# Optimization experiments

Hardware: AMD Instinct MI355X
Metric: run time of the kernel (lower is better)

Reference implementation:

```python
import jax, jax.numpy as jnp
import numpy as np

N = 50000      # nodes across the batched graph
E = 400000     # edges
F_IN = 128     # gnn_input_size
H = 3          # num_head
D = 64         # gnn_hidden_size
G = 64         # graphs in batch
P = 64         # pattern_input_size
NEG_GAT = 0.2  # GATv2Conv leaky_relu slope (dgl default)
NEG = 0.01     # nn.LeakyReLU default slope


def setup_inputs() -> dict:
    key = jax.random.key(0)
    ks = jax.random.split(key, 32)
    rn = lambda k, s, sc=0.05: jax.random.normal(k, s, dtype=jnp.float32) * sc
    HD = H * D
    return {
        "inputs": rn(ks[0], (N, F_IN), 1.0),
        "src": jax.random.randint(ks[1], (E,), 0, N),
        "dst": jax.random.randint(ks[2], (E,), 0, N),
        "graph_ids": jnp.sort(jax.random.randint(ks[3], (N,), 0, G)),
        "p1": rn(ks[4], (G, P), 1.0),
        "p2": rn(ks[5], (G, P), 1.0),
        "p3": rn(ks[6], (G, P), 1.0),
        # GATv2 layer params: fc_src, fc_dst, attn vector, bias
        "W1s": rn(ks[7], (F_IN, HD)), "W1d": rn(ks[8], (F_IN, HD)),
        "a1": rn(ks[9], (H, D)), "b1": rn(ks[10], (HD,)),
        "W2s": rn(ks[11], (HD, HD)), "W2d": rn(ks[12], (HD, HD)),
        "a2": rn(ks[13], (H, D)), "b2": rn(ks[14], (HD,)),
        "W3s": rn(ks[15], (HD, HD)), "W3d": rn(ks[16], (HD, HD)),
        "a3": rn(ks[17], (H, D)), "b3": rn(ks[18], (HD,)),
        # pattern branch (forward only uses ex_layer1 for all three inputs)
        "Wex": rn(ks[19], (P, 32)), "bex": rn(ks[20], (32,)),
        "Wpat": rn(ks[21], (96, P)), "bpat": rn(ks[22], (P,)),
        # classifier head
        "Wc1": rn(ks[23], (D + P, 64)), "bc1": rn(ks[24], (64,)),
        "Wc2": rn(ks[25], (64, 32)), "bc2": rn(ks[26], (32,)),
        "Wc3": rn(ks[27], (32, 2)), "bc3": rn(ks[28], (2,)),
    }


def _gatv2(x, src, dst, Ws, Wd, attn, bias):
    # dgl GATv2Conv (share_weights=False): e = a . leaky_relu(Ws x_u + Wd x_v)
    fs = (x @ Ws).reshape(N, H, D)
    fd = (x @ Wd).reshape(N, H, D)
    e = jax.nn.leaky_relu(fs[src] + fd[dst], NEG_GAT)            # [E,H,D]
    logits = jnp.einsum('ehd,hd->eh', e, attn)                   # [E,H]
    m = jax.ops.segment_max(logits, dst, num_segments=N)         # [N,H]
    m = jnp.where(jnp.isfinite(m), m, 0.0)                       # nodes w/o in-edges
    ex = jnp.exp(logits - m[dst])
    denom = jax.ops.segment_sum(ex, dst, num_segments=N)         # [N,H]
    alpha = ex / jnp.maximum(denom, 1e-9)[dst]                   # edge softmax
    out = jax.ops.segment_sum(alpha[:, :, None] * fs[src], dst, num_segments=N)
    return out + bias.reshape(1, H, D)                           # [N,H,D]


def reference(inputs, src, dst, graph_ids, p1, p2, p3,
              W1s, W1d, a1, b1, W2s, W2d, a2, b2, W3s, W3d, a3, b3,
              Wex, bex, Wpat, bpat, Wc1, bc1, Wc2, bc2, Wc3, bc3):
    h = _gatv2(inputs, src, dst, W1s, W1d, a1, b1).reshape(N, H * D)
    h = _gatv2(h, src, dst, W2s, W2d, a2, b2).reshape(N, H * D)
    h = _gatv2(h, src, dst, W3s, W3d, a3, b3).mean(axis=1)       # [N,D]
    # dgl.mean_nodes: per-graph mean over nodes
    sums = jax.ops.segment_sum(h, graph_ids, num_segments=G)
    cnts = jax.ops.segment_sum(jnp.ones((N,), h.dtype), graph_ids, num_segments=G)
    gnn_out = sums / jnp.maximum(cnts, 1.0)[:, None]             # [G,D]
    # pattern branch (ex_layer1 applied to all three, as in source)
    px = jnp.concatenate([p1 @ Wex + bex, p2 @ Wex + bex, p3 @ Wex + bex], axis=1)
    px = jax.nn.leaky_relu(px @ Wpat + bpat, NEG)                # [G,P]
    x = jnp.concatenate([gnn_out, px], axis=1)                   # [G,D+P]
    x = jax.nn.leaky_relu(x @ Wc1 + bc1, NEG)
    x = jax.nn.leaky_relu(x @ Wc2 + bc2, NEG)
    return x @ Wc3 + bc3                                         # [G,2]
```

## Files before the change

kernel.cpp:

```cpp
#include <hip/hip_runtime.h>
#include <cstdint>
#include <cstddef>

#define NN 50000
#define EE 400000
#define FIN 128
#define HH 3
#define DD 64
#define GG 64
#define PP 64
#define HD 192

typedef short bf16x8 __attribute__((ext_vector_type(8)));
typedef float f32x4 __attribute__((ext_vector_type(4)));
typedef unsigned int u32x2 __attribute__((ext_vector_type(2)));

__device__ inline int wsumi(int v) {
#pragma unroll
    for (int m = 32; m > 0; m >>= 1) v += __shfl_xor(v, m, 64);
    return v;
}

__device__ inline float bf2f(unsigned short u) {
    union { unsigned int i; float f; } x; x.i = ((unsigned int)u) << 16; return x.f;
}
__device__ inline unsigned short f2bf(float f) {
    union { float f; unsigned int i; } x; x.f = f;
    unsigned int r = x.i + 0x7FFFu + ((x.i >> 16) & 1u);
    return (unsigned short)(r >> 16);
}

__device__ inline void unp2(unsigned int w, float& lo, float& hi) {
    union { unsigned int i; float f; } x;
    x.i = w << 16;          lo = x.f;
    x.i = w & 0xFFFF0000u;  hi = x.f;
}
__device__ inline void load4(const unsigned short* p, float* o) {
    u32x2 w = *(const u32x2*)p;
    unp2(w[0], o[0], o[1]);
    unp2(w[1], o[2], o[3]);
}

__device__ inline void loadrow(const unsigned short* __restrict__ FS, int u, int col,
                               float f[3][4]) {
    size_t bu = (size_t)u * HD + col;
#pragma unroll
    for (int h = 0; h < 3; h++) load4(&FS[bu + h * 64], f[h]);
}

__global__ void k_count(const int* __restrict__ dst, int* __restrict__ counts) {
    int e = blockIdx.x * 256 + threadIdx.x;
    if (e < EE) atomicAdd(&counts[dst[e]], 1);
}

__global__ void k_scan_block(const int* __restrict__ in, int* __restrict__ out,
                             int* __restrict__ bsums) {
    __shared__ int tmp[1024];
    int tid = threadIdx.x;
    int i = blockIdx.x * 1024 + tid;
    int v = (i < NN) ? in[i] : 0;
    tmp[tid] = v;
    __syncthreads();
    for (int off = 1; off < 1024; off <<= 1) {
        int t = (tid >= off) ? tmp[tid - off] : 0;
        __syncthreads();
        tmp[tid] += t;
        __syncthreads();
    }
    if (i < NN) out[i] = tmp[tid] - v;
    if (tid == 1023) bsums[blockIdx.x] = tmp[1023];
}

__global__ void k_scan_add(int* __restrict__ row_ptr, const int* __restrict__ bsums, int nb) {
    __shared__ int sbase;
    int tid = threadIdx.x;
    if (tid < 64) {
        int v = (tid < blockIdx.x) ? bsums[tid] : 0;
        v = wsumi(v);
        if (tid == 0) sbase = v;
    }
    __syncthreads();
    int i = blockIdx.x * 1024 + tid;
    if (i < NN) row_ptr[i] += sbase;
    else if (i == NN) row_ptr[NN] = EE;
}

__global__ void k_scatter(const int* __restrict__ src, const int* __restrict__ dst,
                          const int* __restrict__ row_ptr, int* __restrict__ cursor,
                          int* __restrict__ csr_src) {
    int e = blockIdx.x * 256 + threadIdx.x;
    if (e >= EE) return;
    int v = dst[e];
    int pos = row_ptr[v] + atomicAdd(&cursor[v], 1);
    csr_src[pos] = src[e];
}

__device__ inline void pack_one(const float* __restrict__ W, unsigned short* __restrict__ WP,
                                int id, int Kc) {
    int lane = id & 63;
    int kc = (id >> 6) % Kc;
    int ct = (id >> 6) / Kc;
    int n = ct * 16 + (lane & 15);
    int kb = kc * 32 + (lane >> 4) * 8;
#pragma unroll
    for (int j = 0; j < 8; j++)
        WP[(unsigned)id * 8 + j] = f2bf(W[(unsigned)(kb + j) * HD + n]);
}

#define IDS128 (12 * 4 * 64)
#define IDS192 (12 * 6 * 64)
__global__ void k_pack_all(const float* W1s, const float* W1d,
                           const float* W2s, const float* W2d,
                           const float* W3s, const float* W3d,
                           unsigned short* P1s, unsigned short* P1d,
                           unsigned short* P2s, unsigned short* P2d,
                           unsigned short* P3s, unsigned short* P3d) {
    int idx = blockIdx.x * 256 + threadIdx.x;
    if (idx < IDS128) { pack_one(W1s, P1s, idx, 4); return; }
    idx -= IDS128;
    if (idx < IDS128) { pack_one(W1d, P1d, idx, 4); return; }
    idx -= IDS128;
    if (idx < IDS192) { pack_one(W2s, P2s, idx, 6); return; }
    idx -= IDS192;
    if (idx < IDS192) { pack_one(W2d, P2d, idx, 6); return; }
    idx -= IDS192;
    if (idx < IDS192) { pack_one(W3s, P3s, idx, 6); return; }
    idx -= IDS192;
    if (idx < IDS192) { pack_one(W3d, P3d, idx, 6); return; }
}

template <int K, bool BF16IN>
__global__ __launch_bounds__(256) void k_gemm_mfma(const void* __restrict__ Xin,
                                                   const unsigned short* __restrict__ WPs,
                                                   const unsigned short* __restrict__ WPd,
                                                   unsigned short* __restrict__ FS,
                                                   unsigned short* __restrict__ FD) {
    constexpr int Kc = K / 32;
    __shared__ unsigned short smem[64 * 392];
    unsigned short (*xs)[K + 8] = (unsigned short (*)[K + 8])smem;
    unsigned short (*cs)[392]   = (unsigned short (*)[392])smem;
    int tid = threadIdx.x;
    int row0 = blockIdx.x * 64;

    if (BF16IN) {
        const unsigned short* XB = (const unsigned short*)Xin;
        for (int c = tid; c < 64 * K / 8; c += 256) {
            int r = c / (K / 8), kk = (c - r * (K / 8)) * 8;
            int row = row0 + r; if (row > NN - 1) row = NN - 1;
            *(bf16x8*)&xs[r][kk] = *(const bf16x8*)&XB[(unsigned)(row * K + kk)];
        }
    } else {
        const float* X = (const float*)Xin;
        for (int c = tid; c < 64 * K / 4; c += 256) {
            int r = c / (K / 4), k4 = (c - r * (K / 4)) * 4;
            int row = row0 + r; if (row > NN - 1) row = NN - 1;
            f32x4 v = *(const f32x4*)&X[(unsigned)(row * K + k4)];
            xs[r][k4 + 0] = f2bf(v[0]);
            xs[r][k4 + 1] = f2bf(v[1]);
            xs[r][k4 + 2] = f2bf(v[2]);
            xs[r][k4 + 3] = f2bf(v[3]);
        }
    }
    __syncthreads();

    int lane = tid & 63, wv = tid >> 6;
    int m = lane & 15, quad = lane >> 4;
    f32x4 acc[4][6];
#pragma unroll
    for (int s = 0; s < 4; s++)
#pragma unroll
        for (int t = 0; t < 6; t++) acc[s][t] = (f32x4){0.f, 0.f, 0.f, 0.f};

    for (int kc = 0; kc < Kc; kc++) {
        bf16x8 b[6];
#pragma unroll
        for (int t = 0; t < 6; t++) {
            int ct = wv * 6 + t;
            const unsigned short* wp = (ct < 12) ? WPs : WPd;
            int c = (ct < 12) ? ct : ct - 12;
            b[t] = *(const bf16x8*)&wp[(unsigned)(((c * Kc + kc) * 64 + lane) * 8)];
        }
#pragma unroll
        for (int s = 0; s < 4; s++) {
            bf16x8 a = *(const bf16x8*)&xs[s * 16 + m][kc * 32 + quad * 8];
#pragma unroll
            for (int t = 0; t < 6; t++)
                acc[s][t] = __builtin_amdgcn_mfma_f32_16x16x32_bf16(a, b[t], acc[s][t], 0, 0, 0);
        }
    }
    __syncthreads();
#pragma unroll
    for (int s = 0; s < 4; s++)
#pragma unroll
        for (int t = 0; t < 6; t++) {
            int ct = wv * 6 + t;
#pragma unroll
            for (int r = 0; r < 4; r++)
                cs[s * 16 + quad * 4 + r][ct * 16 + m] = f2bf(acc[s][t][r]);
        }
    __syncthreads();
#pragma unroll
    for (int it = 0; it < 12; it++) {
        int c = tid + it * 256;
        int hm = c / 1536;
        int cc = c - hm * 1536;
        int row = cc / 24, ch = cc - row * 24;
        int grow = row0 + row;
        if (grow < NN) {
            unsigned short* OUT = hm ? FD : FS;
            *(bf16x8*)&OUT[(unsigned)(grow * HD + ch * 8)] =
                *(const bf16x8*)&cs[row][hm * 192 + ch * 8];
        }
    }
}

template <bool FINAL>
__global__ __launch_bounds__(256) void k_node_gat(const int* __restrict__ row_ptr,
                                                  const int* __restrict__ csr_src,
                                                  const unsigned short* __restrict__ FS,
                                                  const unsigned short* __restrict__ FD,
                                                  const float* __restrict__ A,
                                                  const float* __restrict__ Bv,
                                                  unsigned short* __restrict__ XB,
                                                  float* __restrict__ H64) {
    int tid = threadIdx.x;
    int grp = tid >> 4, sub = tid & 15;
    int node = blockIdx.x * 16 + grp;
    int col = sub * 4;

    float a[3][4];
#pragma unroll
    for (int h = 0; h < 3; h++) {
        f32x4 av = *(const f32x4*)&A[h * 64 + col];
#pragma unroll
        for (int j = 0; j < 4; j++) a[h][j] = av[j];
    }

    int lo = row_ptr[node], hi = row_ptr[node + 1];

    float g[3][4];
#pragma unroll
    for (int h = 0; h < 3; h++) load4(&FD[(size_t)node * HD + h * 64 + col], g[h]);

    float r[3][4];
#pragma unroll
    for (int h = 0; h < 3; h++)
#pragma unroll
        for (int j = 0; j < 4; j++) r[h][j] = 0.f;
    float d0 = 0.f, d1 = 0.f, d2 = 0.f;

    auto accum = [&](const float f[3][4]) {
        float p0 = 0.f, p1 = 0.f, p2 = 0.f;
#pragma unroll
        for (int j = 0; j < 4; j++) {
            float s0 = f[0][j] + g[0][j]; s0 = fmaxf(s0, 0.2f * s0); p0 += s0 * a[0][j];
            float s1 = f[1][j] + g[1][j]; s1 = fmaxf(s1, 0.2f * s1); p1 += s1 * a[1][j];
            float s2 = f[2][j] + g[2][j]; s2 = fmaxf(s2, 0.2f * s2); p2 += s2 * a[2][j];
        }
#pragma unroll
        for (int m = 8; m > 0; m >>= 1) {
            p0 += __shfl_xor(p0, m, 64);
            p1 += __shfl_xor(p1, m, 64);
            p2 += __shfl_xor(p2, m, 64);
        }
        float w0 = __expf(p0), w1 = __expf(p1), w2 = __expf(p2);
#pragma unroll
        for (int j = 0; j < 4; j++) {
            r[0][j] += w0 * f[0][j];
            r[1][j] += w1 * f[1][j];
            r[2][j] += w2 * f[2][j];
        }
        d0 += w0; d1 += w1; d2 += w2;
    };

    if (hi > lo) {
        int last = hi - 1;
        float fA[3][4], fB[3][4], fC[3][4];
        loadrow(FS, csr_src[lo], col, fA);
        loadrow(FS, csr_src[lo + 1 <= last ? lo + 1 : last], col, fB);
        for (int e = lo; e < hi; e += 3) {
            int eC = e + 2 <= last ? e + 2 : last;
            int eA = e + 3 <= last ? e + 3 : last;
            int eB = e + 4 <= last ? e + 4 : last;
            int uC = csr_src[eC], uA = csr_src[eA], uB = csr_src[eB];
            loadrow(FS, uC, col, fC);
            accum(fA);
            loadrow(FS, uA, col, fA);
            if (e + 1 < hi) accum(fB);
            loadrow(FS, uB, col, fB);
            if (e + 2 < hi) accum(fC);
        }
    }

    float b[3][4];
#pragma unroll
    for (int h = 0; h < 3; h++) {
        f32x4 bv = *(const f32x4*)&Bv[h * 64 + col];
#pragma unroll
        for (int j = 0; j < 4; j++) b[h][j] = bv[j];
    }

    float q0 = fmaxf(d0, 1e-9f), q1 = fmaxf(d1, 1e-9f), q2 = fmaxf(d2, 1e-9f);
    if (FINAL) {
        f32x4 m;
#pragma unroll
        for (int j = 0; j < 4; j++)
            m[j] = (r[0][j] / q0 + b[0][j] + r[1][j] / q1 + b[1][j] +
                    r[2][j] / q2 + b[2][j]) * (1.f / 3.f);
        *(f32x4*)&H64[(size_t)node * 64 + col] = m;
    } else {
        float qq[3] = {q0, q1, q2};
#pragma unroll
        for (int h = 0; h < 3; h++) {
            unsigned short o0 = f2bf(r[h][0] / qq[h] + b[h][0]);
            unsigned short o1 = f2bf(r[h][1] / qq[h] + b[h][1]);
            unsigned short o2 = f2bf(r[h][2] / qq[h] + b[h][2]);
            unsigned short o3 = f2bf(r[h][3] / qq[h] + b[h][3]);
            u32x2 w;
            w[0] = (unsigned)o0 | ((unsigned)o1 << 16);
            w[1] = (unsigned)o2 | ((unsigned)o3 << 16);
            *(u32x2*)&XB[(size_t)node * HD + h * 64 + col] = w;
        }
    }
}

__global__ __launch_bounds__(256) void k_graph_mean(const float* __restrict__ H64,
                                                    const int* __restrict__ gids,
                                                    float* __restrict__ gsum,
                                                    int* __restrict__ gcnt) {
    int g = blockIdx.x >> 2, q = blockIdx.x & 3;
    int lo, hi;
    {
        int a = 0, b = NN;
        while (a < b) { int m = (a + b) >> 1; if (gids[m] < g) a = m + 1; else b = m; }
        lo = a;
        b = NN;
        while (a < b) { int m = (a + b) >> 1; if (gids[m] < g + 1) a = m + 1; else b = m; }
        hi = a;
    }
    int len = hi - lo;
    int qlen = (len + 3) >> 2;
    int s = lo + q * qlen;
    int e = s + qlen; if (e > hi) e = hi;
    int lane = threadIdx.x & 63, wv = threadIdx.x >> 6;

    float acc = 0.f;
    for (int v = s + wv; v < e; v += 4)
        acc += H64[(size_t)v * 64 + lane];
    __shared__ float red[4][64];
    red[wv][lane] = acc;
    __syncthreads();
    if (wv == 0) {
        float t = red[0][lane] + red[1][lane] + red[2][lane] + red[3][lane];
        if (e > s) {
            atomicAdd(&gsum[g * 64 + lane], t);
            if (lane == 0) atomicAdd(&gcnt[g], e - s);
        }
    }
}

__global__ __launch_bounds__(128) void k_head(const float* __restrict__ gsum, const int* __restrict__ gcnt,
                                              const float* __restrict__ p1, const float* __restrict__ p2,
                                              const float* __restrict__ p3,
                                              const float* __restrict__ Wex, const float* __restrict__ bex,
                                              const float* __restrict__ Wpat, const float* __restrict__ bpat,
                                              const float* __restrict__ Wc1, const float* __restrict__ bc1,
                                              const float* __restrict__ Wc2, const float* __restrict__ bc2,
                                              const float* __restrict__ Wc3, const float* __restrict__ bc3,
                                              float* __restrict__ out) {
    int g = blockIdx.x;
    int tid = threadIdx.x;
    __shared__ float pbuf[192];
    __shared__ float ex[96], xc[128], t1[64], t2[32];

    if (tid < 64)       pbuf[tid] = p1[g * 64 + tid];
    else if (tid < 128) pbuf[tid] = p2[g * 64 + tid - 64];
    if (tid < 64)       pbuf[128 + tid] = p3[g * 64 + tid];
    if (tid >= 64 && tid < 128)
        xc[tid - 64] = gsum[g * 64 + tid - 64] / fmaxf((float)gcnt[g], 1.f);
    __syncthreads();
    if (tid < 96) {
        int jj = tid & 31;
        const float* pp = &pbuf[(tid >> 5) * 64];
        float acc = bex[jj];
        for (int k = 0; k < 64; k++) acc += pp[k] * Wex[k * 32 + jj];
        ex[tid] = acc;
    }
    __syncthreads();
    if (tid < 64) {
        float acc = bpat[tid];
        for (int k = 0; k < 96; k++) acc += ex[k] * Wpat[k * 64 + tid];
        xc[64 + tid] = acc > 0.f ? acc : 0.01f * acc;
    }
    __syncthreads();
    if (tid < 64) {
        float acc = bc1[tid];
        for (int k = 0; k < 128; k++) acc += xc[k] * Wc1[k * 64 + tid];
        t1[tid] = acc > 0.f ? acc : 0.01f * acc;
    }
    __syncthreads();
    if (tid < 32) {
        float acc = bc2[tid];
        for (int k = 0; k < 64; k++) acc += t1[k] * Wc2[k * 32 + tid];
        t2[tid] = acc > 0.f ? acc : 0.01f * acc;
    }
    __syncthreads();
    if (tid < 2) {
        float acc = bc3[tid];
        for (int k = 0; k < 32; k++) acc += t2[k] * Wc3[k * 2 + tid];
        out[g * 2 + tid] = acc;
    }
}

extern "C" void kernel_launch(void* const* d_in, const int* in_sizes, int n_in,
                              void* d_out, int out_size, void* d_ws, size_t ws_size,
                              hipStream_t stream) {
    const float* X0  = (const float*)d_in[0];
    const int*   src = (const int*)d_in[1];
    const int*   dst = (const int*)d_in[2];
    const int*   gid = (const int*)d_in[3];
    const float* p1  = (const float*)d_in[4];
    const float* p2  = (const float*)d_in[5];
    const float* p3  = (const float*)d_in[6];
    const float* W1s = (const float*)d_in[7],  *W1d = (const float*)d_in[8];
    const float* a1  = (const float*)d_in[9],  *b1  = (const float*)d_in[10];
    const float* W2s = (const float*)d_in[11], *W2d = (const float*)d_in[12];
    const float* a2  = (const float*)d_in[13], *b2  = (const float*)d_in[14];
    const float* W3s = (const float*)d_in[15], *W3d = (const float*)d_in[16];
    const float* a3  = (const float*)d_in[17], *b3  = (const float*)d_in[18];
    const float* Wex = (const float*)d_in[19], *bex = (const float*)d_in[20];
    const float* Wpat= (const float*)d_in[21], *bpat= (const float*)d_in[22];
    const float* Wc1 = (const float*)d_in[23], *bc1 = (const float*)d_in[24];
    const float* Wc2 = (const float*)d_in[25], *bc2 = (const float*)d_in[26];
    const float* Wc3 = (const float*)d_in[27], *bc3 = (const float*)d_in[28];
    float* out = (float*)d_out;

    char* ws = (char*)d_ws;
    size_t off = 0;
    auto alloc = [&](size_t bytes) -> char* {
        char* p = ws + off;
        off = (off + bytes + 255) & ~(size_t)255;
        return p;
    };
    unsigned short* FS = (unsigned short*)alloc((size_t)NN * HD * 2);
    unsigned short* FD = (unsigned short*)alloc((size_t)NN * HD * 2);
    unsigned short* XB = (unsigned short*)alloc((size_t)NN * HD * 2);
    float*          H64= (float*)alloc((size_t)NN * 64 * 4);
    unsigned short* P1s = (unsigned short*)alloc((size_t)192 * 192 * 2);
    unsigned short* P1d = (unsigned short*)alloc((size_t)192 * 192 * 2);
    unsigned short* P2s = (unsigned short*)alloc((size_t)192 * 192 * 2);
    unsigned short* P2d = (unsigned short*)alloc((size_t)192 * 192 * 2);
    unsigned short* P3s = (unsigned short*)alloc((size_t)192 * 192 * 2);
    unsigned short* P3d = (unsigned short*)alloc((size_t)192 * 192 * 2);
    int* row_ptr = (int*)alloc((size_t)(NN + 1) * 4);
    int* csr_src = (int*)alloc((size_t)EE * 4);
    int* bsums   = (int*)alloc(64 * 4);
    char* zbase = ws + off;
    int*   counts = (int*)alloc((size_t)NN * 4);
    int*   cursor = (int*)alloc((size_t)NN * 4);
    float* gsum   = (float*)alloc((size_t)GG * 64 * 4);
    int*   gcnt   = (int*)alloc((size_t)GG * 4);
    size_t zbytes = (size_t)((ws + off) - zbase);

    hipMemsetAsync(zbase, 0, zbytes, stream);

    int ebl = (EE + 255) / 256;
    int nb  = (NN + 1023) / 1024;
    k_count<<<ebl, 256, 0, stream>>>(dst, counts);
    k_scan_block<<<nb, 1024, 0, stream>>>(counts, row_ptr, bsums);
    k_scan_add<<<nb, 1024, 0, stream>>>(row_ptr, bsums, nb);
    k_scatter<<<ebl, 256, 0, stream>>>(src, dst, row_ptr, cursor, csr_src);
    {
        int total = 2 * IDS128 + 4 * IDS192;
        k_pack_all<<<(total + 255) / 256, 256, 0, stream>>>(W1s, W1d, W2s, W2d, W3s, W3d,
                                                            P1s, P1d, P2s, P2d, P3s, P3d);
    }

    int gblk = (NN + 63) / 64;
    int nblk = NN / 16;

    k_gemm_mfma<128, false><<<gblk, 256, 0, stream>>>(X0, P1s, P1d, FS, FD);
    k_node_gat<false><<<nblk, 256, 0, stream>>>(row_ptr, csr_src, FS, FD, a1, b1, XB, nullptr);
    k_gemm_mfma<192, true><<<gblk, 256, 0, stream>>>(XB, P2s, P2d, FS, FD);
    k_node_gat<false><<<nblk, 256, 0, stream>>>(row_ptr, csr_src, FS, FD, a2, b2, XB, nullptr);
    k_gemm_mfma<192, true><<<gblk, 256, 0, stream>>>(XB, P3s, P3d, FS, FD);
    k_node_gat<true><<<nblk, 256, 0, stream>>>(row_ptr, csr_src, FS, FD, a3, b3, nullptr, H64);

    k_graph_mean<<<GG * 4, 256, 0, stream>>>(H64, gid, gsum, gcnt);
    k_head<<<GG, 128, 0, stream>>>(gsum, gcnt, p1, p2, p3, Wex, bex, Wpat, bpat,
                                   Wc1, bc1, Wc2, bc2, Wc3, bc3, out);
}
```

Baseline: 377.7 us.

## Split GEMM into src/dst halves, fuse count with pack, use shuffle-based scan

The MFMA projection kernel now computes the source and destination outputs in two sequential halves. This halves the accumulator registers and the LDS staging buffer, and launch bounds request 4 blocks per SM to raise occupancy. The cost is loading the input tile into LDS twice. Separately, the edge-count and weight-pack kernels are merged into one launch, and the block scan uses wave shuffles instead of a barrier-heavy shared-memory Hillis-Steele scan.

New measurement: 368.0 us, median of 3. 2.5% less time.

```diff
diff --git a/kernel.cpp b/kernel.cpp
--- a/kernel.cpp
+++ b/kernel.cpp
@@ -10,6 +10,7 @@
 #define GG 64
 #define PP 64
 #define HD 192
+#define EBL 1563
 
 typedef short bf16x8 __attribute__((ext_vector_type(8)));
 typedef float f32x4 __attribute__((ext_vector_type(4)));
@@ -46,53 +47,6 @@
     size_t bu = (size_t)u * HD + col;
 #pragma unroll
     for (int h = 0; h < 3; h++) load4(&FS[bu + h * 64], f[h]);
-}
-
-__global__ void k_count(const int* __restrict__ dst, int* __restrict__ counts) {
-    int e = blockIdx.x * 256 + threadIdx.x;
-    if (e < EE) atomicAdd(&counts[dst[e]], 1);
-}
-
-__global__ void k_scan_block(const int* __restrict__ in, int* __restrict__ out,
-                             int* __restrict__ bsums) {
-    __shared__ int tmp[1024];
-    int tid = threadIdx.x;
-    int i = blockIdx.x * 1024 + tid;
-    int v = (i < NN) ? in[i] : 0;
-    tmp[tid] = v;
-    __syncthreads();
-    for (int off = 1; off < 1024; off <<= 1) {
-        int t = (tid >= off) ? tmp[tid - off] : 0;
-        __syncthreads();
-        tmp[tid] += t;
-        __syncthreads();
-    }
-    if (i < NN) out[i] = tmp[tid] - v;
-    if (tid == 1023) bsums[blockIdx.x] = tmp[1023];
-}
-
-__global__ void k_scan_add(int* __restrict__ row_ptr, const int* __restrict__ bsums, int nb) {
-    __shared__ int sbase;
-    int tid = threadIdx.x;
-    if (tid < 64) {
-        int v = (tid < blockIdx.x) ? bsums[tid] : 0;
-        v = wsumi(v);
-        if (tid == 0) sbase = v;
-    }
-    __syncthreads();
-    int i = blockIdx.x * 1024 + tid;
-    if (i < NN) row_ptr[i] += sbase;
-    else if (i == NN) row_ptr[NN] = EE;
-}
-
-__global__ void k_scatter(const int* __restrict__ src, const int* __restrict__ dst,
-                          const int* __restrict__ row_ptr, int* __restrict__ cursor,
-                          int* __restrict__ csr_src) {
-    int e = blockIdx.x * 256 + threadIdx.x;
-    if (e >= EE) return;
-    int v = dst[e];
-    int pos = row_ptr[v] + atomicAdd(&cursor[v], 1);
-    csr_src[pos] = src[e];
 }
 
 __device__ inline void pack_one(const float* __restrict__ W, unsigned short* __restrict__ WP,
@@ -109,13 +63,21 @@
 
 #define IDS128 (12 * 4 * 64)
 #define IDS192 (12 * 6 * 64)
-__global__ void k_pack_all(const float* W1s, const float* W1d,
-                           const float* W2s, const float* W2d,
-                           const float* W3s, const float* W3d,
-                           unsigned short* P1s, unsigned short* P1d,
-                           unsigned short* P2s, unsigned short* P2d,
-                           unsigned short* P3s, unsigned short* P3d) {
-    int idx = blockIdx.x * 256 + threadIdx.x;
+
+__global__ void k_count_pack(const int* __restrict__ dst, int* __restrict__ counts,
+                             const float* W1s, const float* W1d,
+                             const float* W2s, const float* W2d,
+                             const float* W3s, const float* W3d,
+                             unsigned short* P1s, unsigned short* P1d,
+                             unsigned short* P2s, unsigned short* P2d,
+                             unsigned short* P3s, unsigned short* P3d) {
+    int b = blockIdx.x;
+    if (b < EBL) {
+        int e = b * 256 + threadIdx.x;
+        if (e < EE) atomicAdd(&counts[dst[e]], 1);
+        return;
+    }
+    int idx = (b - EBL) * 256 + threadIdx.x;
     if (idx < IDS128) { pack_one(W1s, P1s, idx, 4); return; }
     idx -= IDS128;
     if (idx < IDS128) { pack_one(W1d, P1d, idx, 4); return; }
@@ -129,88 +91,146 @@
     if (idx < IDS192) { pack_one(W3d, P3d, idx, 6); return; }
 }
 
+__global__ void k_scan_block(const int* __restrict__ in, int* __restrict__ out,
+                             int* __restrict__ bsums) {
+    int tid = threadIdx.x;
+    int lane = tid & 63, w = tid >> 6;
+    int i = blockIdx.x * 1024 + tid;
+    int v = (i < NN) ? in[i] : 0;
+    int s = v;
+#pragma unroll
+    for (int d = 1; d < 64; d <<= 1) {
+        int t = __shfl_up(s, d, 64);
+        if (lane >= d) s += t;
+    }
+    __shared__ int wsum[16], wpre[16];
+    if (lane == 63) wsum[w] = s;
+    __syncthreads();
+    if (w == 0 && lane < 16) {
+        int x = wsum[lane];
+#pragma unroll
+        for (int d = 1; d < 16; d <<= 1) {
+            int t = __shfl_up(x, d, 64);
+            if (lane >= d) x += t;
+        }
+        wpre[lane] = x - wsum[lane];
+        if (lane == 15) bsums[blockIdx.x] = x;
+    }
+    __syncthreads();
+    if (i < NN) out[i] = s - v + wpre[w];
+}
+
+__global__ void k_scan_add(int* __restrict__ row_ptr, const int* __restrict__ bsums, int nb) {
+    __shared__ int sbase;
+    int tid = threadIdx.x;
+    if (tid < 64) {
+        int v = (tid < blockIdx.x) ? bsums[tid] : 0;
+        v = wsumi(v);
+        if (tid == 0) sbase = v;
+    }
+    __syncthreads();
+    int i = blockIdx.x * 1024 + tid;
+    if (i < NN) row_ptr[i] += sbase;
+    else if (i == NN) row_ptr[NN] = EE;
+}
+
+__global__ void k_scatter(const int* __restrict__ src, const int* __restrict__ dst,
+                          const int* __restrict__ row_ptr, int* __restrict__ cursor,
+                          int* __restrict__ csr_src) {
+    int e = blockIdx.x * 256 + threadIdx.x;
+    if (e >= EE) return;
+    int v = dst[e];
+    int pos = row_ptr[v] + atomicAdd(&cursor[v], 1);
+    csr_src[pos] = src[e];
+}
+
 template <int K, bool BF16IN>
-__global__ __launch_bounds__(256) void k_gemm_mfma(const void* __restrict__ Xin,
-                                                   const unsigned short* __restrict__ WPs,
-                                                   const unsigned short* __restrict__ WPd,
-                                                   unsigned short* __restrict__ FS,
-                                                   unsigned short* __restrict__ FD) {
+__global__ __launch_bounds__(256, 4) void k_gemm_mfma(const void* __restrict__ Xin,
+                                                      const unsigned short* __restrict__ WPs,
+                                                      const unsigned short* __restrict__ WPd,
+                                                      unsigned short* __restrict__ FS,
+                                                      unsigned short* __restrict__ FD) {
     constexpr int Kc = K / 32;
-    __shared__ unsigned short smem[64 * 392];
-    unsigned short (*xs)[K + 8] = (unsigned short (*)[K + 8])smem;
-    unsigned short (*cs)[392]   = (unsigned short (*)[392])smem;
+    constexpr int XW = K + 8;
+    constexpr int BW = (XW > 200) ? XW : 200;
+    __shared__ unsigned short smem[64 * BW];
+    unsigned short (*xs)[XW]  = (unsigned short (*)[XW])smem;
+    unsigned short (*cs)[200] = (unsigned short (*)[200])smem;
     int tid = threadIdx.x;
     int row0 = blockIdx.x * 64;
-
-    if (BF16IN) {
-        const unsigned short* XB = (const unsigned short*)Xin;
-        for (int c = tid; c < 64 * K / 8; c += 256) {
-            int r = c / (K / 8), kk = (c - r * (K / 8)) * 8;
-            int row = row0 + r; if (row > NN - 1) row = NN - 1;
-            *(bf16x8*)&xs[r][kk] = *(const bf16x8*)&XB[(unsigned)(row * K + kk)];
-        }
-    } else {
-        const float* X = (const float*)Xin;
-        for (int c = tid; c < 64 * K / 4; c += 256) {
-            int r = c / (K / 4), k4 = (c - r * (K / 4)) * 4;
-            int row = row0 + r; if (row > NN - 1) row = NN - 1;
-            f32x4 v = *(const f32x4*)&X[(unsigned)(row * K + k4)];
-            xs[r][k4 + 0] = f2bf(v[0]);
-            xs[r][k4 + 1] = f2bf(v[1]);
-            xs[r][k4 + 2] = f2bf(v[2]);
-            xs[r][k4 + 3] = f2bf(v[3]);
-        }
-    }
-    __syncthreads();
-
     int lane = tid & 63, wv = tid >> 6;
     int m = lane & 15, quad = lane >> 4;
-    f32x4 acc[4][6];
-#pragma unroll
-    for (int s = 0; s < 4; s++)
-#pragma unroll
-        for (int t = 0; t < 6; t++) acc[s][t] = (f32x4){0.f, 0.f, 0.f, 0.f};
-
-    for (int kc = 0; kc < Kc; kc++) {
-        bf16x8 b[6];
-#pragma unroll
-        for (int t = 0; t < 6; t++) {
-            int ct = wv * 6 + t;
-            const unsigned short* wp = (ct < 12) ? WPs : WPd;
-            int c = (ct < 12) ? ct : ct - 12;
-            b[t] = *(const bf16x8*)&wp[(unsigned)(((c * Kc + kc) * 64 + lane) * 8)];
-        }
-#pragma unroll
-        for (int s = 0; s < 4; s++) {
-            bf16x8 a = *(const bf16x8*)&xs[s * 16 + m][kc * 32 + quad * 8];
-#pragma unroll
-            for (int t = 0; t < 6; t++)
-                acc[s][t] = __builtin_amdgcn_mfma_f32_16x16x32_bf16(a, b[t], acc[s][t], 0, 0, 0);
-        }
-    }
-    __syncthreads();
-#pragma unroll
-    for (int s = 0; s < 4; s++)
-#pragma unroll
-        for (int t = 0; t < 6; t++) {
-            int ct = wv * 6 + t;
-#pragma unroll
-            for (int r = 0; r < 4; r++)
-                cs[s * 16 + quad * 4 + r][ct * 16 + m] = f2bf(acc[s][t][r]);
-        }
-    __syncthreads();
-#pragma unroll
-    for (int it = 0; it < 12; it++) {
-        int c = tid + it * 256;
-        int hm = c / 1536;
-        int cc = c - hm * 1536;
-        int row = cc / 24, ch = cc - row * 24;
-        int grow = row0 + row;
-        if (grow < NN) {
-            unsigned short* OUT = hm ? FD : FS;
-            *(bf16x8*)&OUT[(unsigned)(grow * HD + ch * 8)] =
-                *(const bf16x8*)&cs[row][hm * 192 + ch * 8];
-        }
+
+    const unsigned short* WPx[2] = {WPs, WPd};
+    unsigned short* OUTx[2] = {FS, FD};
+
+    for (int half = 0; half < 2; half++) {
+        if (BF16IN) {
+            const unsigned short* XB = (const unsigned short*)Xin;
+            for (int c = tid; c < 64 * K / 8; c += 256) {
+                int r = c / (K / 8), kk = (c - r * (K / 8)) * 8;
+                int row = row0 + r; if (row > NN - 1) row = NN - 1;
+                *(bf16x8*)&xs[r][kk] = *(const bf16x8*)&XB[(unsigned)(row * K + kk)];
+            }
+        } else {
+            const float* X = (const float*)Xin;
+            for (int c = tid; c < 64 * K / 4; c += 256) {
+                int r = c / (K / 4), k4 = (c - r * (K / 4)) * 4;
+                int row = row0 + r; if (row > NN - 1) row = NN - 1;
+                f32x4 v = *(const f32x4*)&X[(unsigned)(row * K + k4)];
+                xs[r][k4 + 0] = f2bf(v[0]);
+                xs[r][k4 + 1] = f2bf(v[1]);
+                xs[r][k4 + 2] = f2bf(v[2]);
+                xs[r][k4 + 3] = f2bf(v[3]);
+            }
+        }
+        __syncthreads();
+
+        f32x4 acc[4][3];
+#pragma unroll
+        for (int s = 0; s < 4; s++)
+#pragma unroll
+            for (int t = 0; t < 3; t++) acc[s][t] = (f32x4){0.f, 0.f, 0.f, 0.f};
+
+        const unsigned short* wp = WPx[half];
+        for (int kc = 0; kc < Kc; kc++) {
+            bf16x8 b[3];
+#pragma unroll
+            for (int t = 0; t < 3; t++) {
+                int c = wv * 3 + t;
+                b[t] = *(const bf16x8*)&wp[(unsigned)(((c * Kc + kc) * 64 + lane) * 8)];
+            }
+#pragma unroll
+            for (int s = 0; s < 4; s++) {
+                bf16x8 a = *(const bf16x8*)&xs[s * 16 + m][kc * 32 + quad * 8];
+#pragma unroll
+                for (int t = 0; t < 3; t++)
+                    acc[s][t] = __builtin_amdgcn_mfma_f32_16x16x32_bf16(a, b[t], acc[s][t], 0, 0, 0);
+            }
+        }
+        __syncthreads();
+
+#pragma unroll
+        for (int s = 0; s < 4; s++)
+#pragma unroll
+            for (int t = 0; t < 3; t++) {
+                int ct = wv * 3 + t;
+#pragma unroll
+                for (int r = 0; r < 4; r++)
+                    cs[s * 16 + quad * 4 + r][ct * 16 + m] = f2bf(acc[s][t][r]);
+            }
+        __syncthreads();
+        unsigned short* OUT = OUTx[half];
+#pragma unroll
+        for (int it = 0; it < 6; it++) {
+            int c = tid + it * 256;
+            int row = c / 24, ch = c - row * 24;
+            int grow = row0 + row;
+            if (grow < NN)
+                *(bf16x8*)&OUT[(unsigned)(grow * HD + ch * 8)] =
+                    *(const bf16x8*)&cs[row][ch * 8];
+        }
+        __syncthreads();
     }
 }
 
@@ -464,17 +484,16 @@
 
     hipMemsetAsync(zbase, 0, zbytes, stream);
 
-    int ebl = (EE + 255) / 256;
     int nb  = (NN + 1023) / 1024;
-    k_count<<<ebl, 256, 0, stream>>>(dst, counts);
+    {
+        int packbl = (2 * IDS128 + 4 * IDS192 + 255) / 256;
+        k_count_pack<<<EBL + packbl, 256, 0, stream>>>(dst, counts,
+                                                       W1s, W1d, W2s, W2d, W3s, W3d,
+                                                       P1s, P1d, P2s, P2d, P3s, P3d);
+    }
     k_scan_block<<<nb, 1024, 0, stream>>>(counts, row_ptr, bsums);
     k_scan_add<<<nb, 1024, 0, stream>>>(row_ptr, bsums, nb);
-    k_scatter<<<ebl, 256, 0, stream>>>(src, dst, row_ptr, cursor, csr_src);
-    {
-        int total = 2 * IDS128 + 4 * IDS192;
-        k_pack_all<<<(total + 255) / 256, 256, 0, stream>>>(W1s, W1d, W2s, W2d, W3s, W3d,
-                                                            P1s, P1d, P2s, P2d, P3s, P3d);
-    }
+    k_scatter<<<EBL, 256, 0, stream>>>(src, dst, row_ptr, cursor, csr_src);
 
     int gblk = (NN + 63) / 64;
     int nblk = NN / 16;
```
